# Kernel tuning notes

Measured on AMD Instinct MI355X. Metric: run time of the kernel, lower is better.

The kernel has to match this reference:

```python
import jax, jax.numpy as jnp
import numpy as np

B, N_IN, N_OUT = 16, 7000, 28000
C_IN, C_OUT, S = 64, 64, 9
NNZ = 3 * N_OUT  # ~3 source verts per upsampled vert (barycentric)


def setup_inputs() -> dict:
    key = jax.random.key(0)
    k = jax.random.split(key, 6)
    x = jax.random.normal(k[0], (B, N_IN, C_IN), dtype=jnp.float32)
    values = jax.random.uniform(k[1], (NNZ,), dtype=jnp.float32)
    row = jax.random.randint(k[2], (NNZ,), 0, N_OUT)
    col = jax.random.randint(k[3], (NNZ,), 0, N_IN)
    spiral_indices = jax.random.randint(k[4], (N_OUT, S), 0, N_OUT)
    weight = jax.random.normal(k[5], (S * C_IN, C_OUT), dtype=jnp.float32) * 0.02
    bias = jnp.zeros((C_OUT,), dtype=jnp.float32)
    return {"x": x, "values": values, "weight": weight, "bias": bias,
            "row": row, "col": col, "spiral_indices": spiral_indices}


def reference(x, values, weight, bias, row, col, spiral_indices):
    # Pool: gather source verts, scale by sparse matrix values, scatter-add to output verts
    n_out = spiral_indices.shape[0]
    gathered = x[:, col, :] * values[None, :, None]            # [B, nnz, C]
    pooled = jnp.zeros((x.shape[0], n_out, x.shape[2]), x.dtype).at[:, row, :].add(gathered)  # [B, N_out, C]
    # SpiralConv: gather spiral neighborhood, flatten, linear
    feat = pooled[:, spiral_indices.reshape(-1), :]            # [B, N_out*S, C]
    feat = feat.reshape(x.shape[0], n_out, -1)                 # [B, N_out, S*C]
    out = jax.nn.elu(jnp.einsum('bnf,fo->bno', feat, weight) + bias)
    return out
```

## Files before the change

kernel.cpp:

```cpp
#include <hip/hip_runtime.h>
#include <math.h>

#define B      16
#define N_IN   7000
#define N_OUT  28000
#define C      64
#define S      9
#define NNZ    (3 * N_OUT)
#define F      (S * C)
#define KB     (F / 32)

typedef short bf16x8 __attribute__((ext_vector_type(8)));
typedef float f32x4  __attribute__((ext_vector_type(4)));

static __device__ __forceinline__ unsigned short f2bf(float f) {
    unsigned u = __float_as_uint(f);
    u += 0x7fffu + ((u >> 16) & 1u);
    return (unsigned short)(u >> 16);
}
static __device__ __forceinline__ float bf2f(unsigned short s) {
    return __uint_as_float((unsigned)s << 16);
}

#define XBF_BLOCKS  3500
#define HIST_BLOCKS 329
#define PACK_BLOCKS 18

__global__ void prep_kernel(const float* __restrict__ x, unsigned short* __restrict__ xb,
                            const float* __restrict__ w, unsigned short* __restrict__ pw,
                            const int*   __restrict__ row, int* __restrict__ cnt) {
    const int blk = blockIdx.x;
    const int tid = threadIdx.x;
    if (blk < XBF_BLOCKS) {
        const size_t i = ((size_t)blk * 256 + tid) * 8;
        const float4 a = *(const float4*)(x + i);
        const float4 c = *(const float4*)(x + i + 4);
        ushort4 o0, o1;
        o0.x = f2bf(a.x); o0.y = f2bf(a.y); o0.z = f2bf(a.z); o0.w = f2bf(a.w);
        o1.x = f2bf(c.x); o1.y = f2bf(c.y); o1.z = f2bf(c.z); o1.w = f2bf(c.w);
        *(ushort4*)(xb + i)     = o0;
        *(ushort4*)(xb + i + 4) = o1;
    } else if (blk < XBF_BLOCKS + HIST_BLOCKS) {
        const int i = (blk - XBF_BLOCKS) * 256 + tid;
        if (i < NNZ) atomicAdd(&cnt[row[i]], 1);
    } else {
        const int kb   = blk - (XBF_BLOCKS + HIST_BLOCKS);
        const int nt   = tid >> 6;
        const int lane = tid & 63;
        const int lm   = lane & 15;
        const int quad = lane >> 4;
        unsigned short v[8];
        #pragma unroll
        for (int j = 0; j < 8; ++j) {
            const int k = kb * 32 + quad * 8 + j;
            const int n = nt * 16 + lm;
            v[j] = f2bf(w[(size_t)k * C + n]);
        }
        unsigned short* dst = pw + ((size_t)(kb * 4 + nt) * 64 + lane) * 8;
        #pragma unroll
        for (int j = 0; j < 8; ++j) dst[j] = v[j];
    }
}

__global__ void scan_kernel(const int* __restrict__ cnt,
                            int* __restrict__ offs, int* __restrict__ cursor) {
    __shared__ int wsum[16];
    __shared__ int carry;
    const int t = threadIdx.x, lane = t & 63, wid = t >> 6;
    if (t == 0) carry = 0;
    __syncthreads();
    int lastTot = 0;
    #pragma unroll 1
    for (int chunk = 0; chunk < 28; ++chunk) {
        const int idx = chunk * 1024 + t;
        const int v = (idx < N_OUT) ? cnt[idx] : 0;
        const int cin = carry;
        int sc = v;
        #pragma unroll
        for (int d = 1; d < 64; d <<= 1) {
            int u = __shfl_up(sc, d, 64);
            if (lane >= d) sc += u;
        }
        if (lane == 63) wsum[wid] = sc;
        __syncthreads();
        int wexcl = 0;
        #pragma unroll
        for (int wj = 0; wj < 15; ++wj)
            wexcl += (wj < wid) ? wsum[wj] : 0;
        const int excl = cin + wexcl + sc - v;
        if (idx < N_OUT) { offs[idx] = excl; cursor[idx] = excl; }
        if (t == 1023) { lastTot = cin + wexcl + sc; carry = lastTot; }
        __syncthreads();
    }
    if (t == 1023) offs[N_OUT] = lastTot;
}

__global__ void place_kernel(const int* __restrict__ row, const int* __restrict__ col,
                             const float* __restrict__ values,
                             int* __restrict__ cursor,
                             int* __restrict__ ecol, float* __restrict__ eval) {
    int i = blockIdx.x * 256 + threadIdx.x;
    if (i < NNZ) {
        int pos = atomicAdd(&cursor[row[i]], 1);
        ecol[pos] = col[i];
        eval[pos] = values[i];
    }
}

__global__ void pool_kernel(const unsigned short* __restrict__ xb,
                            const int*   __restrict__ ecol,
                            const float* __restrict__ eval,
                            const int*   __restrict__ offs,
                            unsigned short* __restrict__ pooled) {
    const int bg     = blockIdx.x & 7;
    const int rowblk = blockIdx.x >> 3;
    const int wave = threadIdx.x >> 6;
    const int lane = threadIdx.x & 63;
    const int rsub = lane >> 5;
    const int bsub = (lane >> 4) & 1;
    const int sl   = lane & 15;

    const int r = rowblk * 8 + wave * 2 + rsub;
    const int b = bg + 8 * bsub;

    const int start = offs[r], end = offs[r + 1];

    float4 acc = make_float4(0.f, 0.f, 0.f, 0.f);
    const unsigned short* xbb = xb + (size_t)b * N_IN * C + sl * 4;

    for (int e = start; e < end; e += 4) {
        const int nn = end - e;
        int   cl[4]; float vv[4];
        #pragma unroll
        for (int j = 0; j < 4; ++j) {
            const int ee = (j < nn) ? e + j : e;
            cl[j] = ecol[ee];
            vv[j] = (j < nn) ? eval[ee] : 0.f;
        }
        ushort4 xv[4];
        #pragma unroll
        for (int j = 0; j < 4; ++j)
            xv[j] = *(const ushort4*)(xbb + (size_t)cl[j] * C);
        #pragma unroll
        for (int j = 0; j < 4; ++j) {
            acc.x = fmaf(bf2f(xv[j].x), vv[j], acc.x);
            acc.y = fmaf(bf2f(xv[j].y), vv[j], acc.y);
            acc.z = fmaf(bf2f(xv[j].z), vv[j], acc.z);
            acc.w = fmaf(bf2f(xv[j].w), vv[j], acc.w);
        }
    }

    unsigned long long ov =
        (unsigned long long)f2bf(acc.x)
        | ((unsigned long long)f2bf(acc.y) << 16)
        | ((unsigned long long)f2bf(acc.z) << 32)
        | ((unsigned long long)f2bf(acc.w) << 48);
    unsigned short* dst = pooled + (size_t)bsub * (N_OUT * 512)
                        + (size_t)r * 512 + bg * 64 + sl * 4;
    __builtin_nontemporal_store(ov, (unsigned long long*)dst);
}

#define BARRIER_NODRAIN() do {                                   \
    asm volatile("s_waitcnt lgkmcnt(0)" ::: "memory");           \
    __builtin_amdgcn_s_barrier();                                \
} while (0)

__global__ __launch_bounds__(512, 4)
void spiral_mfma(const unsigned short* __restrict__ pooled,
                 const bf16x8*         __restrict__ packedW,
                 const int*            __restrict__ sp,
                 const float*          __restrict__ bias,
                 float*                __restrict__ out) {
    const int Lb    = blockIdx.x;
    const int g     = Lb & 1;
    const int mtile = Lb >> 1;
    const int tid   = threadIdx.x;
    const int wave  = tid >> 6;
    const int lane  = tid & 63;
    const int lm    = lane & 15;
    const int quad  = lane >> 4;
    const int m_base = mtile * 32;
    const int b      = g * 8 + wave;

    __shared__ unsigned short apool[2][32][512];
    __shared__ bf16x8         bstage[2][512];

    int spv[S];
    {
        const int r = m_base + (lane & 31);
        #pragma unroll
        for (int s = 0; s < S; ++s) spv[s] = sp[r * S + s];
    }

    const unsigned short* pgbase = pooled + (size_t)g * (N_OUT * 512);

    f32x4 acc[2][4];
    #pragma unroll
    for (int t = 0; t < 2; ++t)
        #pragma unroll
        for (int nt = 0; nt < 4; ++nt)
            acc[t][nt] = (f32x4){0.f, 0.f, 0.f, 0.f};

    bf16x8 ldA2[2][4];
    bf16x8 ldB2[2];

    #pragma unroll
    for (int q = 0; q < 4; ++q) {
        const int r = __shfl(spv[0], wave * 4 + q, 64);
        ldA2[0][q] = *(const bf16x8*)(pgbase + (size_t)r * 512 + lane * 8);
    }
    ldB2[0] = packedW[tid];
    #pragma unroll
    for (int q = 0; q < 4; ++q) {
        const int r = __shfl(spv[1], wave * 4 + q, 64);
        ldA2[1][q] = *(const bf16x8*)(pgbase + (size_t)r * 512 + lane * 8);
    }
    ldB2[1] = packedW[512 + tid];
    #pragma unroll
    for (int q = 0; q < 4; ++q) {
        const int j = wave * 4 + q;
        *(bf16x8*)(&apool[0][j][(lane ^ (j & 7)) * 8]) = ldA2[0][q];
    }
    bstage[0][tid] = ldB2[0];
    BARRIER_NODRAIN();

    #pragma unroll
    for (int s = 0; s < S; ++s) {
        const int cur = s & 1, nxt = cur ^ 1;

        if (s + 2 < S) {
            #pragma unroll
            for (int q = 0; q < 4; ++q) {
                const int r = __shfl(spv[s + 2], wave * 4 + q, 64);
                ldA2[s & 1][q] = *(const bf16x8*)(pgbase + (size_t)r * 512 + lane * 8);
            }
            ldB2[s & 1] = packedW[(s + 2) * 512 + tid];
        }

        #pragma unroll
        for (int half = 0; half < 2; ++half) {
            bf16x8 bb[4];
            #pragma unroll
            for (int nt = 0; nt < 4; ++nt)
                bb[nt] = bstage[cur][(half * 4 + nt) * 64 + lane];
            bf16x8 aa[2];
            #pragma unroll
            for (int t = 0; t < 2; ++t) {
                const int j = t * 16 + lm;
                const int chunk = wave * 8 + (((half * 4 + quad) ^ (j & 7)));
                aa[t] = *(const bf16x8*)(&apool[cur][j][chunk * 8]);
            }
            #pragma unroll
            for (int nt = 0; nt < 4; ++nt)
                #pragma unroll
                for (int t = 0; t < 2; ++t)
                    acc[t][nt] = __builtin_amdgcn_mfma_f32_16x16x32_bf16(
                        aa[t], bb[nt], acc[t][nt], 0, 0, 0);
        }

        if (s + 1 < S) {
            #pragma unroll
            for (int q = 0; q < 4; ++q) {
                const int j = wave * 4 + q;
                *(bf16x8*)(&apool[nxt][j][(lane ^ (j & 7)) * 8]) = ldA2[(s + 1) & 1][q];
            }
            bstage[nxt][tid] = ldB2[(s + 1) & 1];
        }
        BARRIER_NODRAIN();
    }

    #pragma unroll
    for (int nt = 0; nt < 4; ++nt) {
        const int n = nt * 16 + lm;
        const float bs = bias[n];
        #pragma unroll
        for (int t = 0; t < 2; ++t) {
            #pragma unroll
            for (int reg = 0; reg < 4; ++reg) {
                const int r = m_base + t * 16 + quad * 4 + reg;
                float v = acc[t][nt][reg] + bs;
                v = v > 0.f ? v : (__expf(v) - 1.0f);
                __builtin_nontemporal_store(v,
                    out + ((size_t)b * N_OUT + r) * C + n);
            }
        }
    }
}

extern "C" void kernel_launch(void* const* d_in, const int* in_sizes, int n_in,
                              void* d_out, int out_size, void* d_ws, size_t ws_size,
                              hipStream_t stream) {
    const float* x      = (const float*)d_in[0];
    const float* values = (const float*)d_in[1];
    const float* weight = (const float*)d_in[2];
    const float* bias   = (const float*)d_in[3];
    const int*   row    = (const int*)d_in[4];
    const int*   col    = (const int*)d_in[5];
    const int*   sp     = (const int*)d_in[6];
    float*       out    = (float*)d_out;

    char* ws = (char*)d_ws;
    size_t off = 0;
    unsigned short* pooled  = (unsigned short*)(ws + off); off += (size_t)B * N_OUT * C * 2;
    unsigned short* packedW = (unsigned short*)(ws + off); off += (size_t)KB * 4 * 64 * 8 * 2;
    unsigned short* xbf     = (unsigned short*)(ws + off); off += (size_t)B * N_IN * C * 2;
    int*   offs   = (int*)(ws + off); off += ((size_t)(N_OUT + 1) * 4 + 124) / 128 * 128;
    int*   cursor = (int*)(ws + off); off += (size_t)N_OUT * 4 + 128;
    int*   cnt    = (int*)(ws + off); off += (size_t)N_OUT * 4 + 128;
    int*   ecol   = (int*)(ws + off); off += (size_t)NNZ * 4;
    float* eval   = (float*)(ws + off); off += (size_t)NNZ * 4;

    (void)hipMemsetAsync(cnt, 0, (size_t)N_OUT * 4, stream);

    prep_kernel<<<XBF_BLOCKS + HIST_BLOCKS + PACK_BLOCKS, 256, 0, stream>>>(
        x, xbf, weight, packedW, row, cnt);

    scan_kernel<<<1, 1024, 0, stream>>>(cnt, offs, cursor);

    place_kernel<<<(NNZ + 255) / 256, 256, 0, stream>>>(row, col, values, cursor, ecol, eval);

    pool_kernel<<<3500 * 8, 256, 0, stream>>>(xbf, ecol, eval, offs, pooled);

    spiral_mfma<<<875 * 2, 512, 0, stream>>>(pooled,
        reinterpret_cast<const bf16x8*>(packedW), sp, bias, out);
}
```

Baseline: 303.2 us.

## Fuse histogram into single-block scan, deepen spiral prefetch, raise MFMA priority

Moves the row histogram out of prep_kernel into a single-block kernel that counts into a 28000-entry LDS array before doing the prefix scan. This drops the memset and the global atomics, at the cost of having one block run 84k LDS atomics serially. In the spiral MFMA kernel, global prefetch of gathered rows and weights now runs three steps ahead instead of two, which uses more registers. It also wraps the MFMA sequence in s_setprio so the matrix math gets issue priority.

```diff
diff --git a/kernel.cpp b/kernel.cpp
--- a/kernel.cpp
+++ b/kernel.cpp
@@ -23,12 +23,10 @@
 }
 
 #define XBF_BLOCKS  3500
-#define HIST_BLOCKS 329
 #define PACK_BLOCKS 18
 
 __global__ void prep_kernel(const float* __restrict__ x, unsigned short* __restrict__ xb,
-                            const float* __restrict__ w, unsigned short* __restrict__ pw,
-                            const int*   __restrict__ row, int* __restrict__ cnt) {
+                            const float* __restrict__ w, unsigned short* __restrict__ pw) {
     const int blk = blockIdx.x;
     const int tid = threadIdx.x;
     if (blk < XBF_BLOCKS) {
@@ -40,11 +38,8 @@
         o1.x = f2bf(c.x); o1.y = f2bf(c.y); o1.z = f2bf(c.z); o1.w = f2bf(c.w);
         *(ushort4*)(xb + i)     = o0;
         *(ushort4*)(xb + i + 4) = o1;
-    } else if (blk < XBF_BLOCKS + HIST_BLOCKS) {
-        const int i = (blk - XBF_BLOCKS) * 256 + tid;
-        if (i < NNZ) atomicAdd(&cnt[row[i]], 1);
     } else {
-        const int kb   = blk - (XBF_BLOCKS + HIST_BLOCKS);
+        const int kb   = blk - XBF_BLOCKS;
         const int nt   = tid >> 6;
         const int lane = tid & 63;
         const int lm   = lane & 15;
@@ -62,19 +57,23 @@
     }
 }
 
-__global__ void scan_kernel(const int* __restrict__ cnt,
-                            int* __restrict__ offs, int* __restrict__ cursor) {
+__global__ void histscan_kernel(const int* __restrict__ row,
+                                int* __restrict__ offs, int* __restrict__ cursor) {
+    __shared__ int h[N_OUT];
     __shared__ int wsum[16];
-    __shared__ int carry;
     const int t = threadIdx.x, lane = t & 63, wid = t >> 6;
-    if (t == 0) carry = 0;
+
+    #pragma unroll
+    for (int j = t; j < N_OUT; j += 1024) h[j] = 0;
     __syncthreads();
-    int lastTot = 0;
+    for (int i = t; i < NNZ; i += 1024) atomicAdd(&h[row[i]], 1);
+    __syncthreads();
+
+    int carry = 0;
     #pragma unroll 1
     for (int chunk = 0; chunk < 28; ++chunk) {
         const int idx = chunk * 1024 + t;
-        const int v = (idx < N_OUT) ? cnt[idx] : 0;
-        const int cin = carry;
+        const int v = (idx < N_OUT) ? h[idx] : 0;
         int sc = v;
         #pragma unroll
         for (int d = 1; d < 64; d <<= 1) {
@@ -83,16 +82,19 @@
         }
         if (lane == 63) wsum[wid] = sc;
         __syncthreads();
-        int wexcl = 0;
-        #pragma unroll
-        for (int wj = 0; wj < 15; ++wj)
-            wexcl += (wj < wid) ? wsum[wj] : 0;
-        const int excl = cin + wexcl + sc - v;
+        int wexcl = 0, tot = 0;
+        #pragma unroll
+        for (int wj = 0; wj < 16; ++wj) {
+            const int s = wsum[wj];
+            wexcl += (wj < wid) ? s : 0;
+            tot   += s;
+        }
+        const int excl = carry + wexcl + sc - v;
         if (idx < N_OUT) { offs[idx] = excl; cursor[idx] = excl; }
-        if (t == 1023) { lastTot = cin + wexcl + sc; carry = lastTot; }
+        carry += tot;
         __syncthreads();
     }
-    if (t == 1023) offs[N_OUT] = lastTot;
+    if (t == 0) offs[N_OUT] = carry;
 }
 
 __global__ void place_kernel(const int* __restrict__ row, const int* __restrict__ col,
@@ -201,40 +203,37 @@
         for (int nt = 0; nt < 4; ++nt)
             acc[t][nt] = (f32x4){0.f, 0.f, 0.f, 0.f};
 
-    bf16x8 ldA2[2][4];
-    bf16x8 ldB2[2];
-
-    #pragma unroll
-    for (int q = 0; q < 4; ++q) {
-        const int r = __shfl(spv[0], wave * 4 + q, 64);
-        ldA2[0][q] = *(const bf16x8*)(pgbase + (size_t)r * 512 + lane * 8);
-    }
-    ldB2[0] = packedW[tid];
-    #pragma unroll
-    for (int q = 0; q < 4; ++q) {
-        const int r = __shfl(spv[1], wave * 4 + q, 64);
-        ldA2[1][q] = *(const bf16x8*)(pgbase + (size_t)r * 512 + lane * 8);
-    }
-    ldB2[1] = packedW[512 + tid];
+    bf16x8 ldA3[3][4];
+    bf16x8 ldB3[3];
+
+    #pragma unroll
+    for (int k = 0; k < 3; ++k) {
+        #pragma unroll
+        for (int q = 0; q < 4; ++q) {
+            const int r = __shfl(spv[k], wave * 4 + q, 64);
+            ldA3[k][q] = *(const bf16x8*)(pgbase + (size_t)r * 512 + lane * 8);
+        }
+        ldB3[k] = packedW[k * 512 + tid];
+    }
     #pragma unroll
     for (int q = 0; q < 4; ++q) {
         const int j = wave * 4 + q;
-        *(bf16x8*)(&apool[0][j][(lane ^ (j & 7)) * 8]) = ldA2[0][q];
-    }
-    bstage[0][tid] = ldB2[0];
+        *(bf16x8*)(&apool[0][j][(lane ^ (j & 7)) * 8]) = ldA3[0][q];
+    }
+    bstage[0][tid] = ldB3[0];
     BARRIER_NODRAIN();
 
     #pragma unroll
     for (int s = 0; s < S; ++s) {
         const int cur = s & 1, nxt = cur ^ 1;
 
-        if (s + 2 < S) {
+        if (s + 3 < S) {
             #pragma unroll
             for (int q = 0; q < 4; ++q) {
-                const int r = __shfl(spv[s + 2], wave * 4 + q, 64);
-                ldA2[s & 1][q] = *(const bf16x8*)(pgbase + (size_t)r * 512 + lane * 8);
+                const int r = __shfl(spv[s + 3], wave * 4 + q, 64);
+                ldA3[s % 3][q] = *(const bf16x8*)(pgbase + (size_t)r * 512 + lane * 8);
             }
-            ldB2[s & 1] = packedW[(s + 2) * 512 + tid];
+            ldB3[s % 3] = packedW[(s + 3) * 512 + tid];
         }
 
         #pragma unroll
@@ -250,21 +249,23 @@
                 const int chunk = wave * 8 + (((half * 4 + quad) ^ (j & 7)));
                 aa[t] = *(const bf16x8*)(&apool[cur][j][chunk * 8]);
             }
+            __builtin_amdgcn_s_setprio(1);
             #pragma unroll
             for (int nt = 0; nt < 4; ++nt)
                 #pragma unroll
                 for (int t = 0; t < 2; ++t)
                     acc[t][nt] = __builtin_amdgcn_mfma_f32_16x16x32_bf16(
                         aa[t], bb[nt], acc[t][nt], 0, 0, 0);
+            __builtin_amdgcn_s_setprio(0);
         }
 
         if (s + 1 < S) {
             #pragma unroll
             for (int q = 0; q < 4; ++q) {
                 const int j = wave * 4 + q;
-                *(bf16x8*)(&apool[nxt][j][(lane ^ (j & 7)) * 8]) = ldA2[(s + 1) & 1][q];
+                *(bf16x8*)(&apool[nxt][j][(lane ^ (j & 7)) * 8]) = ldA3[(s + 1) % 3][q];
             }
-            bstage[nxt][tid] = ldB2[(s + 1) & 1];
+            bstage[nxt][tid] = ldB3[(s + 1) % 3];
         }
         BARRIER_NODRAIN();
     }
@@ -306,16 +307,12 @@
     unsigned short* xbf     = (unsigned short*)(ws + off); off += (size_t)B * N_IN * C * 2;
     int*   offs   = (int*)(ws + off); off += ((size_t)(N_OUT + 1) * 4 + 124) / 128 * 128;
     int*   cursor = (int*)(ws + off); off += (size_t)N_OUT * 4 + 128;
-    int*   cnt    = (int*)(ws + off); off += (size_t)N_OUT * 4 + 128;
     int*   ecol   = (int*)(ws + off); off += (size_t)NNZ * 4;
     float* eval   = (float*)(ws + off); off += (size_t)NNZ * 4;
 
-    (void)hipMemsetAsync(cnt, 0, (size_t)N_OUT * 4, stream);
-
-    prep_kernel<<<XBF_BLOCKS + HIST_BLOCKS + PACK_BLOCKS, 256, 0, stream>>>(
-        x, xbf, weight, packedW, row, cnt);
-
-    scan_kernel<<<1, 1024, 0, stream>>>(cnt, offs, cursor);
+    prep_kernel<<<XBF_BLOCKS + PACK_BLOCKS, 256, 0, stream>>>(x, xbf, weight, packedW);
+
+    histscan_kernel<<<1, 1024, 0, stream>>>(row, offs, cursor);
 
     place_kernel<<<(NNZ + 255) / 256, 256, 0, stream>>>(row, col, values, cursor, ecol, eval);
 
```

Result: slower. 423.1 us (+39.6%).
